# Optimization experiments

Measured on AMD Instinct MI355X. Metric: run time of the kernel, lower is better.

Reference implementation:

```python
import jax, jax.numpy as jnp
import numpy as np


def _rbf(X1, X2, log_ls):
    # exp(-||x1-x2||^2 / (2*ls^2)) via the squared-norm expansion
    sq1 = jnp.sum(X1 * X1, axis=-1)[:, None]
    sq2 = jnp.sum(X2 * X2, axis=-1)[None, :]
    d2 = jnp.maximum(sq1 + sq2 - 2.0 * (X1 @ X2.T), 0.0)
    ls2 = jnp.exp(2.0 * log_ls)
    return jnp.exp(-d2 / (2.0 * ls2))


def setup_inputs() -> dict:
    key = jax.random.key(0)
    k1, k2, k3 = jax.random.split(key, 3)
    N_way, K_shot, Q_query, D = 16, 32, 4096, 1024
    Zs = jax.random.normal(k1, (N_way * K_shot, D), dtype=jnp.float32)
    Ys = jax.random.randint(k2, (N_way * K_shot, 1), 0, N_way)
    Zq = jax.random.normal(k3, (N_way * Q_query, D), dtype=jnp.float32)
    log_ls = jnp.asarray(0.0, dtype=jnp.float32)
    log_noise = jnp.asarray(-3.0, dtype=jnp.float32)
    return {"Zs": Zs, "Ys": Ys, "Zq": Zq, "log_ls": log_ls,
            "log_noise": log_noise, "N_way": N_way}


def reference(Zs, Ys, Zq, log_ls, log_noise, N_way):
    Nsamp = Zs.shape[0]  # N_way * K_shot
    Y1hot = jax.nn.one_hot(Ys.reshape(-1), N_way, dtype=Zs.dtype)  # [Nsamp, N_way]
    noise = jnp.exp(2.0 * log_noise)
    Kss = _rbf(Zs, Zs, log_ls) + noise * jnp.eye(Nsamp, dtype=Zs.dtype)
    L = jnp.linalg.cholesky(Kss)
    alpha = jax.scipy.linalg.cho_solve((L, True), Y1hot)  # [Nsamp, N_way]
    Kqs = _rbf(Zq, Zs, log_ls)  # [Q, Nsamp]
    f_q = Kqs @ alpha  # [Q, N_way]
    return jax.nn.softmax(f_q, axis=-1)
```

## Files before the change

kernel.cpp:

```cpp
#include <hip/hip_runtime.h>
#include <math.h>

#define NS 512
#define NQ 65536
#define DD 1024
#define NW 16

typedef __attribute__((ext_vector_type(8))) short short8x;
typedef __attribute__((ext_vector_type(4))) float floatx4;

static __device__ __forceinline__ unsigned short bf_trunc(float x) {
  return (unsigned short)(__float_as_uint(x) >> 16);
}
static __device__ __forceinline__ float bf_tof(unsigned short h) {
  return __uint_as_float(((unsigned)h) << 16);
}
static __device__ __forceinline__ unsigned short bf_rne(float x) {
  unsigned u = __float_as_uint(x);
  return (unsigned short)((u + 0x7FFFu + ((u >> 16) & 1u)) >> 16);
}

#define STASH(Hp, Lp, row, k0, v) do {                                      \
    unsigned e_ = (unsigned)((((row) * 32 + (k0)) ^ (((row) & 7) << 3)));   \
    ushort4 h_, l_;                                                         \
    h_.x = bf_trunc((v).x); l_.x = bf_trunc((v).x - bf_tof(h_.x));          \
    h_.y = bf_trunc((v).y); l_.y = bf_trunc((v).y - bf_tof(h_.y));          \
    h_.z = bf_trunc((v).z); l_.z = bf_trunc((v).z - bf_tof(h_.z));          \
    h_.w = bf_trunc((v).w); l_.w = bf_trunc((v).w - bf_tof(h_.w));          \
    *(ushort4*)&Hp[e_] = h_; *(ushort4*)&Lp[e_] = l_;                       \
  } while (0)

__global__ void row_norms_kernel(const float* __restrict__ X, float* __restrict__ out, int nrows) {
  int gw = (int)((blockIdx.x * blockDim.x + threadIdx.x) >> 6);
  int lane = threadIdx.x & 63;
  if (gw >= nrows) return;
  const float* row = X + (size_t)gw * DD;
  float s = 0.f;
  #pragma unroll
  for (int i = 0; i < 4; ++i) {
    float4 v = *(const float4*)(row + 4 * lane + 256 * i);
    s += v.x * v.x + v.y * v.y + v.z * v.z + v.w * v.w;
  }
  #pragma unroll
  for (int off = 32; off; off >>= 1) s += __shfl_xor(s, off);
  if (lane == 0) out[gw] = s;
}

__global__ __launch_bounds__(256) void kss_kernel(const float* __restrict__ Zs,
                                                  const float* __restrict__ sn,
                                                  const float* __restrict__ log_ls,
                                                  const float* __restrict__ log_noise,
                                                  float* __restrict__ K) {
  __shared__ __align__(16) float At[16][68];
  __shared__ __align__(16) float Bt[16][68];
  int tid = threadIdx.x;
  int rb = blockIdx.y * 64, cb = blockIdx.x * 64;
  int tx = tid & 15, ty = tid >> 4;
  int srow = tid & 63, skq = (tid >> 6) << 2;
  float acc[4][4] = {};
  for (int kk = 0; kk < DD; kk += 16) {
    __syncthreads();
    float4 a = *(const float4*)(Zs + (size_t)(rb + srow) * DD + kk + skq);
    float4 b = *(const float4*)(Zs + (size_t)(cb + srow) * DD + kk + skq);
    At[skq + 0][srow] = a.x; At[skq + 1][srow] = a.y; At[skq + 2][srow] = a.z; At[skq + 3][srow] = a.w;
    Bt[skq + 0][srow] = b.x; Bt[skq + 1][srow] = b.y; Bt[skq + 2][srow] = b.z; Bt[skq + 3][srow] = b.w;
    __syncthreads();
    #pragma unroll
    for (int k = 0; k < 16; ++k) {
      float4 av = *(const float4*)&At[k][ty * 4];
      float4 bv = *(const float4*)&Bt[k][tx * 4];
      float aa[4] = {av.x, av.y, av.z, av.w};
      float bb[4] = {bv.x, bv.y, bv.z, bv.w};
      #pragma unroll
      for (int i = 0; i < 4; ++i)
        #pragma unroll
        for (int j = 0; j < 4; ++j)
          acc[i][j] = fmaf(aa[i], bb[j], acc[i][j]);
    }
  }
  float inv2 = 0.5f * expf(-2.f * log_ls[0]);
  float noise = expf(2.f * log_noise[0]);
  #pragma unroll
  for (int i = 0; i < 4; ++i)
    #pragma unroll
    for (int j = 0; j < 4; ++j) {
      int r = rb + ty * 4 + i, c = cb + tx * 4 + j;
      float d2 = fmaxf(sn[r] + sn[c] - 2.f * acc[i][j], 0.f);
      float v = expf(-d2 * inv2);
      if (r == c) v += noise;
      K[(size_t)r * NS + c] = v;
    }
}

__global__ __launch_bounds__(512) void chol_panel(float* __restrict__ K, int j) {
  __shared__ float A[64][65];
  __shared__ float diag[64], idia[64];
  int tid = threadIdx.x;
  for (int i = tid; i < 4096; i += 512) {
    int r = i >> 6, c = i & 63;
    A[r][c] = K[(size_t)(j + r) * NS + j + c];
  }
  __syncthreads();
  for (int c = 0; c < 64; ++c) {
    float d = A[c][c];
    float s = sqrtf(d);
    float inv = 1.f / s;
    if (tid == c) { diag[c] = s; idia[c] = inv; }
    if (tid < 64 && tid > c) A[tid][c] *= inv;
    __syncthreads();
    for (int i = tid; i < 4096; i += 512) {
      int r = i >> 6, k = i & 63;
      if (r > c && k > c) A[r][k] -= A[r][c] * A[k][c];
    }
    __syncthreads();
  }
  for (int i = tid; i < 4096; i += 512) {
    int r = i >> 6, c = i & 63;
    if (c <= r) K[(size_t)(j + r) * NS + j + c] = (c == r) ? diag[r] : A[r][c];
  }
  for (int r0 = j + 64 + tid; r0 < NS; r0 += 512) {
    float x[64];
    #pragma unroll
    for (int c = 0; c < 64; ++c) {
      float v = K[(size_t)r0 * NS + j + c];
      #pragma unroll
      for (int k = 0; k < c; ++k) v -= x[k] * A[c][k];
      x[c] = v * idia[c];
    }
    #pragma unroll
    for (int c = 0; c < 64; ++c) K[(size_t)r0 * NS + j + c] = x[c];
  }
}

__global__ __launch_bounds__(256) void syrk_trailing(float* __restrict__ K, int j) {
  int t0 = j + 64;
  int rbt = t0 + blockIdx.y * 64, cbt = t0 + blockIdx.x * 64;
  if (cbt > rbt) return;
  __shared__ float A[64][69];
  __shared__ float B[64][69];
  int tid = threadIdx.x;
  for (int i = tid; i < 64 * 64; i += 256) {
    int r = i >> 6, k = i & 63;
    A[r][k] = K[(size_t)(rbt + r) * NS + j + k];
    B[r][k] = K[(size_t)(cbt + r) * NS + j + k];
  }
  __syncthreads();
  int tx = tid & 15, ty = tid >> 4;
  float acc[4][4] = {};
  for (int k = 0; k < 64; ++k) {
    float aa[4], bb[4];
    #pragma unroll
    for (int i = 0; i < 4; ++i) aa[i] = A[ty * 4 + i][k];
    #pragma unroll
    for (int i = 0; i < 4; ++i) bb[i] = B[tx * 4 + i][k];
    #pragma unroll
    for (int i = 0; i < 4; ++i)
      #pragma unroll
      for (int jj = 0; jj < 4; ++jj)
        acc[i][jj] = fmaf(aa[i], bb[jj], acc[i][jj]);
  }
  #pragma unroll
  for (int i = 0; i < 4; ++i)
    #pragma unroll
    for (int jj = 0; jj < 4; ++jj)
      K[(size_t)(rbt + ty * 4 + i) * NS + cbt + tx * 4 + jj] -= acc[i][jj];
}

__global__ __launch_bounds__(256) void transpose_fill(float* __restrict__ K) {
  int bx = blockIdx.x, by = blockIdx.y;
  if (by < bx) return;
  int rb = by * 64, cb = bx * 64;
  __shared__ float T[64][65];
  int tid = threadIdx.x;
  int rr = tid >> 4, pc = (tid & 15) * 4;
  #pragma unroll
  for (int u = 0; u < 4; ++u) {
    int r = rr + 16 * u;
    *(float4*)&T[r][pc] = *(const float4*)(K + (size_t)(rb + r) * NS + cb + pc);
  }
  __syncthreads();
  if (by == bx) {
    #pragma unroll
    for (int u = 0; u < 4; ++u) {
      int r = rr + 16 * u;
      #pragma unroll
      for (int i = 0; i < 4; ++i) {
        int c = pc + i;
        if (c > r) K[(size_t)(rb + r) * NS + cb + c] = T[c][r];
      }
    }
  } else {
    #pragma unroll
    for (int u = 0; u < 4; ++u) {
      int orr = rr + 16 * u;
      float4 o;
      o.x = T[pc + 0][orr]; o.y = T[pc + 1][orr];
      o.z = T[pc + 2][orr]; o.w = T[pc + 3][orr];
      *(float4*)(K + (size_t)(cb + orr) * NS + rb + pc) = o;
    }
  }
}

__global__ __launch_bounds__(1024) void cho_solve_v2(const float* __restrict__ K,
                                                     const int* __restrict__ Ys,
                                                     unsigned short* __restrict__ alpha_t) {
  __shared__ float P[64][68];
  __shared__ float WsT[16][68];
  __shared__ float Wblk[64][16];
  __shared__ float invd[64];
  const int tid = threadIdx.x;
  const int rs = tid >> 4, nn = tid & 15;
  const int pc = nn * 4;

  float w[8];
  #pragma unroll
  for (int k = 0; k < 8; ++k) w[k] = (Ys[rs + 64 * k] == nn) ? 1.f : 0.f;

  for (int jb = 0; jb < 8; ++jb) {
    const int j = jb << 6;
    __syncthreads();
    #pragma unroll
    for (int k = 0; k < 8; ++k) if (k == jb) Wblk[rs][nn] = w[k];
    *(floatx4*)&P[rs][pc] = *(const floatx4*)(K + (size_t)(j + rs) * NS + j + pc);
    __syncthreads();
    if (tid < 64) {
      const int n = tid & 15, rq = tid >> 4;
      invd[tid] = 1.f / P[tid][tid];
      float w16[16];
      #pragma unroll
      for (int i = 0; i < 16; ++i) w16[i] = Wblk[rq + 4 * i][n];
      #pragma unroll
      for (int g = 0; g < 16; ++g) {
        floatx4 p[16];
        #pragma unroll
        for (int i = 0; i < 16; ++i) p[i] = *(const floatx4*)&P[rq + 4 * i][4 * g];
        #pragma unroll
        for (int cj = 0; cj < 4; ++cj) {
          const int c = 4 * g + cj;
          float xc = __shfl(w16[c >> 2], ((c & 3) << 4) + n) * invd[c];
          if (rq == (c & 3)) w16[c >> 2] = xc;
          #pragma unroll
          for (int i = 0; i < 16; ++i) {
            int r = rq + 4 * i;
            if (r > c) w16[i] -= p[i][cj] * xc;
          }
        }
      }
      #pragma unroll
      for (int i = 0; i < 16; ++i) WsT[n][rq + 4 * i] = w16[i];
    }
    __syncthreads();
    #pragma unroll
    for (int k = 0; k < 8; ++k) if (k == jb) w[k] = WsT[nn][rs];
    floatx4 wsr[16];
    #pragma unroll
    for (int g = 0; g < 16; ++g) wsr[g] = *(const floatx4*)&WsT[nn][4 * g];
    #pragma unroll
    for (int k = 0; k < 8; ++k) {
      if (k > jb) {
        const float* lrow = K + (size_t)(rs + 64 * k) * NS + j;
        float s = w[k];
        #pragma unroll
        for (int g = 0; g < 16; ++g) {
          floatx4 lv = *(const floatx4*)(lrow + 4 * g);
          s -= lv.x * wsr[g].x + lv.y * wsr[g].y + lv.z * wsr[g].z + lv.w * wsr[g].w;
        }
        w[k] = s;
      }
    }
  }

  for (int jb = 7; jb >= 0; --jb) {
    const int j = jb << 6;
    __syncthreads();
    #pragma unroll
    for (int k = 0; k < 8; ++k) if (k == jb) Wblk[rs][nn] = w[k];
    *(floatx4*)&P[rs][pc] = *(const floatx4*)(K + (size_t)(j + rs) * NS + j + pc);
    __syncthreads();
    if (tid < 64) {
      const int n = tid & 15, rq = tid >> 4;
      invd[tid] = 1.f / P[tid][tid];
      float w16[16];
      #pragma unroll
      for (int i = 0; i < 16; ++i) w16[i] = Wblk[rq + 4 * i][n];
      #pragma unroll
      for (int g = 15; g >= 0; --g) {
        floatx4 p[16];
        #pragma unroll
        for (int i = 0; i < 16; ++i) p[i] = *(const floatx4*)&P[rq + 4 * i][4 * g];
        #pragma unroll
        for (int cj = 3; cj >= 0; --cj) {
          const int c = 4 * g + cj;
          float xc = __shfl(w16[c >> 2], ((c & 3) << 4) + n) * invd[c];
          if (rq == (c & 3)) w16[c >> 2] = xc;
          #pragma unroll
          for (int i = 0; i < 16; ++i) {
            int r = rq + 4 * i;
            if (r < c) w16[i] -= p[i][cj] * xc;
          }
        }
      }
      #pragma unroll
      for (int i = 0; i < 16; ++i) WsT[n][rq + 4 * i] = w16[i];
    }
    __syncthreads();
    #pragma unroll
    for (int k = 0; k < 8; ++k) if (k == jb) w[k] = WsT[nn][rs];
    floatx4 wsr[16];
    #pragma unroll
    for (int g = 0; g < 16; ++g) wsr[g] = *(const floatx4*)&WsT[nn][4 * g];
    #pragma unroll
    for (int k = 0; k < 8; ++k) {
      if (k < jb) {
        const float* lrow = K + (size_t)(rs + 64 * k) * NS + j;
        float s = w[k];
        #pragma unroll
        for (int g = 0; g < 16; ++g) {
          floatx4 lv = *(const floatx4*)(lrow + 4 * g);
          s -= lv.x * wsr[g].x + lv.y * wsr[g].y + lv.z * wsr[g].z + lv.w * wsr[g].w;
        }
        w[k] = s;
      }
    }
  }

  #pragma unroll
  for (int k = 0; k < 8; ++k)
    alpha_t[(size_t)nn * NS + rs + 64 * k] = bf_rne(w[k]);
}

__global__ __launch_bounds__(512) void fused_v2(const float* __restrict__ Zq,
                                                const float* __restrict__ Zs,
                                                const float* __restrict__ sn,
                                                const unsigned short* __restrict__ alpha_t,
                                                const float* __restrict__ log_ls,
                                                float* __restrict__ out) {
  __shared__ __align__(16) unsigned short LB[32768];
  __shared__ float qnl[128];
  __shared__ float snl[256];
  unsigned short* AhB = LB;
  unsigned short* AlB = LB + 4096;
  unsigned short* BhB = LB + 8192;
  unsigned short* BlB = LB + 16384;
  unsigned short* KqB = LB;

  const int tid = threadIdx.x;
  const int lane = tid & 63;
  const int w = tid >> 6;
  const int wm = w >> 2, wn = w & 3;
  const int l15 = lane & 15, l4 = lane >> 4;
  const int rb = blockIdx.x * 128;
  const float inv2 = 0.5f * __expf(-2.f * log_ls[0]);
  const unsigned swz = (unsigned)((l15 & 7) << 3);

  if (tid < 128) qnl[tid] = 0.f;
  __syncthreads();

  const int qrow0 = tid >> 3;
  const int qk0 = (tid & 7) * 4;
  const int qrow1 = 64 + qrow0;

  floatx4 facc = {0.f, 0.f, 0.f, 0.f};

  for (int cc = 0; cc < NS; cc += 256) {
    if (tid < 256) snl[tid] = sn[cc + tid];
    floatx4 acc[4][4];
    #pragma unroll
    for (int a = 0; a < 4; ++a)
      #pragma unroll
      for (int b = 0; b < 4; ++b) acc[a][b] = (floatx4){0.f, 0.f, 0.f, 0.f};

    float4 pq0 = *(const float4*)(Zq + (size_t)(rb + qrow0) * DD + qk0);
    float4 pq1 = *(const float4*)(Zq + (size_t)(rb + qrow1) * DD + qk0);
    float4 ps[4];
    #pragma unroll
    for (int u = 0; u < 4; ++u) {
      int idx = tid + (u << 9);
      ps[u] = *(const float4*)(Zs + (size_t)(cc + (idx >> 3)) * DD + ((idx & 7) * 4));
    }

    for (int kt = 0; kt < 32; ++kt) {
      STASH(AhB, AlB, qrow0, qk0, pq0);
      STASH(AhB, AlB, qrow1, qk0, pq1);
      #pragma unroll
      for (int u = 0; u < 4; ++u) {
        int idx = tid + (u << 9);
        int srow = idx >> 3, sk0 = (idx & 7) * 4;
        STASH(BhB, BlB, srow, sk0, ps[u]);
      }
      if (cc == 0) {
        float s0 = pq0.x * pq0.x + pq0.y * pq0.y + pq0.z * pq0.z + pq0.w * pq0.w;
        float s1 = pq1.x * pq1.x + pq1.y * pq1.y + pq1.z * pq1.z + pq1.w * pq1.w;
        #pragma unroll
        for (int d = 1; d < 8; d <<= 1) { s0 += __shfl_xor(s0, d); s1 += __shfl_xor(s1, d); }
        if ((tid & 7) == 0) { qnl[qrow0] += s0; qnl[qrow1] += s1; }
      }
      __syncthreads();
      if (kt < 31) {
        int kk2 = (kt + 1) << 5;
        pq0 = *(const float4*)(Zq + (size_t)(rb + qrow0) * DD + kk2 + qk0);
        pq1 = *(const float4*)(Zq + (size_t)(rb + qrow1) * DD + kk2 + qk0);
        #pragma unroll
        for (int u = 0; u < 4; ++u) {
          int idx = tid + (u << 9);
          ps[u] = *(const float4*)(Zs + (size_t)(cc + (idx >> 3)) * DD + kk2 + ((idx & 7) * 4));
        }
      }
      short8x ah[4], al[4], bh[4], bl[4];
      #pragma unroll
      for (int mi = 0; mi < 4; ++mi) {
        unsigned e = (unsigned)((wm * 64 + mi * 16 + l15) * 32 + 8 * l4) ^ swz;
        ah[mi] = *(const short8x*)&AhB[e];
        al[mi] = *(const short8x*)&AlB[e];
      }
      #pragma unroll
      for (int ni = 0; ni < 4; ++ni) {
        unsigned e = (unsigned)((wn * 64 + ni * 16 + l15) * 32 + 8 * l4) ^ swz;
        bh[ni] = *(const short8x*)&BhB[e];
        bl[ni] = *(const short8x*)&BlB[e];
      }
      #pragma unroll
      for (int mi = 0; mi < 4; ++mi)
        #pragma unroll
        for (int ni = 0; ni < 4; ++ni) {
          acc[mi][ni] = __builtin_amdgcn_mfma_f32_16x16x32_bf16(ah[mi], bh[ni], acc[mi][ni], 0, 0, 0);
          acc[mi][ni] = __builtin_amdgcn_mfma_f32_16x16x32_bf16(ah[mi], bl[ni], acc[mi][ni], 0, 0, 0);
          acc[mi][ni] = __builtin_amdgcn_mfma_f32_16x16x32_bf16(al[mi], bh[ni], acc[mi][ni], 0, 0, 0);
        }
      __syncthreads();
    }

    short8x bfr[8];
    #pragma unroll
    for (int s = 0; s < 8; ++s)
      bfr[s] = *(const short8x*)(alpha_t + ((size_t)l15 * NS + cc + 32 * s + 8 * l4));

    #pragma unroll
    for (int mi = 0; mi < 4; ++mi)
      #pragma unroll
      for (int rr = 0; rr < 4; ++rr) {
        int row_l = wm * 64 + mi * 16 + l4 * 4 + rr;
        float qv = qnl[row_l];
        unsigned sw = (unsigned)((row_l & 7) << 3);
        #pragma unroll
        for (int ni = 0; ni < 4; ++ni) {
          int col = wn * 64 + ni * 16 + l15;
          float d2 = fmaxf(qv + snl[col] - 2.f * acc[mi][ni][rr], 0.f);
          float kq = __expf(-d2 * inv2);
          KqB[(unsigned)(row_l * 256 + col) ^ sw] = bf_rne(kq);
        }
      }
    __syncthreads();
    #pragma unroll
    for (int s = 0; s < 8; ++s) {
      unsigned e = (unsigned)((w * 16 + l15) * 256 + 32 * s + 8 * l4) ^ swz;
      short8x ak = *(const short8x*)&KqB[e];
      facc = __builtin_amdgcn_mfma_f32_16x16x32_bf16(ak, bfr[s], facc, 0, 0, 0);
    }
    __syncthreads();
  }

  #pragma unroll
  for (int r = 0; r < 4; ++r) {
    float v = facc[r];
    float m = v;
    #pragma unroll
    for (int d = 1; d < 16; d <<= 1) m = fmaxf(m, __shfl_xor(m, d));
    float e = __expf(v - m);
    float s = e;
    #pragma unroll
    for (int d = 1; d < 16; d <<= 1) s += __shfl_xor(s, d);
    out[(size_t)(rb + w * 16 + l4 * 4 + r) * NW + l15] = e / s;
  }
}

extern "C" void kernel_launch(void* const* d_in, const int* in_sizes, int n_in,
                              void* d_out, int out_size, void* d_ws, size_t ws_size,
                              hipStream_t stream) {
  (void)in_sizes; (void)n_in; (void)out_size; (void)ws_size;
  const float* Zs = (const float*)d_in[0];
  const int*   Ys = (const int*)d_in[1];
  const float* Zq = (const float*)d_in[2];
  const float* log_ls = (const float*)d_in[3];
  const float* log_noise = (const float*)d_in[4];
  float* out = (float*)d_out;

  float* ws = (float*)d_ws;
  float* K  = ws;
  float* sn = ws + (size_t)NS * NS;
  unsigned short* alpha_t = (unsigned short*)(sn + NS);

  row_norms_kernel<<<128, 256, 0, stream>>>(Zs, sn, NS);
  kss_kernel<<<dim3(8, 8), 256, 0, stream>>>(Zs, sn, log_ls, log_noise, K);
  for (int j = 0; j < NS; j += 64) {
    chol_panel<<<1, 512, 0, stream>>>(K, j);
    int rows = NS - j - 64;
    if (rows > 0) {
      int t = rows / 64;
      syrk_trailing<<<dim3(t, t), 256, 0, stream>>>(K, j);
    }
  }
  transpose_fill<<<dim3(8, 8), 256, 0, stream>>>(K);
  cho_solve_v2<<<1, 1024, 0, stream>>>(K, Ys, alpha_t);
  fused_v2<<<NQ / 128, 512, 0, stream>>>(Zq, Zs, sn, alpha_t, log_ls, out);
}
```

Before: 1.404 ms.

## Fuse blocked Cholesky, trailing update, transpose and solve into one single-block kernel

Replaces the per-panel chol_panel/syrk_trailing launch sequence, the transpose_fill pass and the separate solve with one 1024-thread single-block kernel. The diagonal factorization is done by one wavefront using register rows and shuffles, and the transposed upper triangle is written as it is produced. This removes about 17 kernel launches and their gaps. In exchange, the trailing SYRK updates now run serially on a single CU instead of across many blocks, and they are tightly synchronized.

Result: slower. 1.570 ms (+11.8%).

```diff
diff --git a/kernel.cpp b/kernel.cpp
--- a/kernel.cpp
+++ b/kernel.cpp
@@ -92,126 +92,108 @@
     }
 }
 
-__global__ __launch_bounds__(512) void chol_panel(float* __restrict__ K, int j) {
-  __shared__ float A[64][65];
-  __shared__ float diag[64], idia[64];
-  int tid = threadIdx.x;
-  for (int i = tid; i < 4096; i += 512) {
-    int r = i >> 6, c = i & 63;
-    A[r][c] = K[(size_t)(j + r) * NS + j + c];
-  }
-  __syncthreads();
-  for (int c = 0; c < 64; ++c) {
-    float d = A[c][c];
-    float s = sqrtf(d);
-    float inv = 1.f / s;
-    if (tid == c) { diag[c] = s; idia[c] = inv; }
-    if (tid < 64 && tid > c) A[tid][c] *= inv;
-    __syncthreads();
-    for (int i = tid; i < 4096; i += 512) {
-      int r = i >> 6, k = i & 63;
-      if (r > c && k > c) A[r][k] -= A[r][c] * A[k][c];
-    }
-    __syncthreads();
-  }
-  for (int i = tid; i < 4096; i += 512) {
-    int r = i >> 6, c = i & 63;
-    if (c <= r) K[(size_t)(j + r) * NS + j + c] = (c == r) ? diag[r] : A[r][c];
-  }
-  for (int r0 = j + 64 + tid; r0 < NS; r0 += 512) {
-    float x[64];
-    #pragma unroll
-    for (int c = 0; c < 64; ++c) {
-      float v = K[(size_t)r0 * NS + j + c];
-      #pragma unroll
-      for (int k = 0; k < c; ++k) v -= x[k] * A[c][k];
-      x[c] = v * idia[c];
-    }
-    #pragma unroll
-    for (int c = 0; c < 64; ++c) K[(size_t)r0 * NS + j + c] = x[c];
-  }
-}
-
-__global__ __launch_bounds__(256) void syrk_trailing(float* __restrict__ K, int j) {
-  int t0 = j + 64;
-  int rbt = t0 + blockIdx.y * 64, cbt = t0 + blockIdx.x * 64;
-  if (cbt > rbt) return;
-  __shared__ float A[64][69];
-  __shared__ float B[64][69];
-  int tid = threadIdx.x;
-  for (int i = tid; i < 64 * 64; i += 256) {
-    int r = i >> 6, k = i & 63;
-    A[r][k] = K[(size_t)(rbt + r) * NS + j + k];
-    B[r][k] = K[(size_t)(cbt + r) * NS + j + k];
-  }
-  __syncthreads();
-  int tx = tid & 15, ty = tid >> 4;
-  float acc[4][4] = {};
-  for (int k = 0; k < 64; ++k) {
-    float aa[4], bb[4];
-    #pragma unroll
-    for (int i = 0; i < 4; ++i) aa[i] = A[ty * 4 + i][k];
-    #pragma unroll
-    for (int i = 0; i < 4; ++i) bb[i] = B[tx * 4 + i][k];
-    #pragma unroll
-    for (int i = 0; i < 4; ++i)
-      #pragma unroll
-      for (int jj = 0; jj < 4; ++jj)
-        acc[i][jj] = fmaf(aa[i], bb[jj], acc[i][jj]);
-  }
-  #pragma unroll
-  for (int i = 0; i < 4; ++i)
-    #pragma unroll
-    for (int jj = 0; jj < 4; ++jj)
-      K[(size_t)(rbt + ty * 4 + i) * NS + cbt + tx * 4 + jj] -= acc[i][jj];
-}
-
-__global__ __launch_bounds__(256) void transpose_fill(float* __restrict__ K) {
-  int bx = blockIdx.x, by = blockIdx.y;
-  if (by < bx) return;
-  int rb = by * 64, cb = bx * 64;
-  __shared__ float T[64][65];
-  int tid = threadIdx.x;
-  int rr = tid >> 4, pc = (tid & 15) * 4;
-  #pragma unroll
-  for (int u = 0; u < 4; ++u) {
-    int r = rr + 16 * u;
-    *(float4*)&T[r][pc] = *(const float4*)(K + (size_t)(rb + r) * NS + cb + pc);
-  }
-  __syncthreads();
-  if (by == bx) {
-    #pragma unroll
-    for (int u = 0; u < 4; ++u) {
-      int r = rr + 16 * u;
-      #pragma unroll
-      for (int i = 0; i < 4; ++i) {
-        int c = pc + i;
-        if (c > r) K[(size_t)(rb + r) * NS + cb + c] = T[c][r];
-      }
-    }
-  } else {
-    #pragma unroll
-    for (int u = 0; u < 4; ++u) {
-      int orr = rr + 16 * u;
-      float4 o;
-      o.x = T[pc + 0][orr]; o.y = T[pc + 1][orr];
-      o.z = T[pc + 2][orr]; o.w = T[pc + 3][orr];
-      *(float4*)(K + (size_t)(cb + orr) * NS + rb + pc) = o;
-    }
-  }
-}
-
-__global__ __launch_bounds__(1024) void cho_solve_v2(const float* __restrict__ K,
-                                                     const int* __restrict__ Ys,
-                                                     unsigned short* __restrict__ alpha_t) {
+__global__ __launch_bounds__(1024) void chol_all(float* __restrict__ K,
+                                                 const int* __restrict__ Ys,
+                                                 unsigned short* __restrict__ alpha_t) {
+  __shared__ float A[64][68];
+  __shared__ float SA[64][65];
+  __shared__ float SBt[64][68];
+  __shared__ float idia[64];
   __shared__ float P[64][68];
   __shared__ float WsT[16][68];
   __shared__ float Wblk[64][16];
   __shared__ float invd[64];
   const int tid = threadIdx.x;
+
+  for (int jb = 0; jb < 8; ++jb) {
+    const int j = jb << 6;
+    __syncthreads();
+    if (tid < 64) {
+      const int r = tid;
+      float ar[64];
+      #pragma unroll
+      for (int c4 = 0; c4 < 16; ++c4)
+        *(floatx4*)&ar[c4 * 4] = *(const floatx4*)(K + (size_t)(j + r) * NS + j + c4 * 4);
+      float myinv = 0.f;
+      #pragma unroll
+      for (int c = 0; c < 64; ++c) {
+        float colv = ar[c];
+        float d = __shfl(colv, c);
+        float sq = sqrtf(d);
+        float inv = 1.f / sq;
+        float x = (r > c) ? colv * inv : ((r == c) ? sq : 0.f);
+        ar[c] = x;
+        if (r == c) myinv = inv;
+        #pragma unroll
+        for (int k = c + 1; k < 64; ++k) {
+          float xk = __shfl(x, k);
+          ar[k] = fmaf(-x, xk, ar[k]);
+        }
+      }
+      idia[r] = myinv;
+      #pragma unroll
+      for (int c = 0; c < 64; ++c) {
+        if (c <= r) {
+          A[r][c] = ar[c];
+          K[(size_t)(j + r) * NS + j + c] = ar[c];
+        }
+        if (c < r) K[(size_t)(j + c) * NS + j + r] = ar[c];
+      }
+    }
+    __syncthreads();
+    {
+      const int r0 = j + 64 + tid;
+      if (r0 < NS) {
+        float x[64];
+        #pragma unroll
+        for (int c = 0; c < 64; ++c) {
+          float v = K[(size_t)r0 * NS + j + c];
+          #pragma unroll
+          for (int k = 0; k < c; ++k) v = fmaf(-x[k], A[c][k], v);
+          x[c] = v * idia[c];
+        }
+        #pragma unroll
+        for (int c = 0; c < 64; ++c) {
+          K[(size_t)r0 * NS + j + c] = x[c];
+          K[(size_t)(j + c) * NS + r0] = x[c];
+        }
+      }
+    }
+    const int T = 7 - jb;
+    for (int ti = 0; ti < T; ++ti)
+      for (int tj = 0; tj <= ti; ++tj) {
+        const int rbt = j + 64 + ti * 64, cbt = j + 64 + tj * 64;
+        __syncthreads();
+        {
+          const int rr = tid >> 4, k4 = (tid & 15) * 4;
+          floatx4 av = *(const floatx4*)(K + (size_t)(rbt + rr) * NS + j + k4);
+          floatx4 bv = *(const floatx4*)(K + (size_t)(cbt + rr) * NS + j + k4);
+          SA[rr][k4 + 0] = av.x; SA[rr][k4 + 1] = av.y;
+          SA[rr][k4 + 2] = av.z; SA[rr][k4 + 3] = av.w;
+          SBt[k4 + 0][rr] = bv.x; SBt[k4 + 1][rr] = bv.y;
+          SBt[k4 + 2][rr] = bv.z; SBt[k4 + 3][rr] = bv.w;
+        }
+        __syncthreads();
+        {
+          const int ty = tid & 63, cg = tid >> 6;
+          floatx4 acc = {0.f, 0.f, 0.f, 0.f};
+          #pragma unroll 8
+          for (int k = 0; k < 64; ++k) {
+            float a = SA[ty][k];
+            floatx4 b = *(const floatx4*)&SBt[k][cg * 4];
+            acc.x = fmaf(a, b.x, acc.x); acc.y = fmaf(a, b.y, acc.y);
+            acc.z = fmaf(a, b.z, acc.z); acc.w = fmaf(a, b.w, acc.w);
+          }
+          float* cp = K + (size_t)(rbt + ty) * NS + cbt + cg * 4;
+          floatx4 cv = *(const floatx4*)cp;
+          cv.x -= acc.x; cv.y -= acc.y; cv.z -= acc.z; cv.w -= acc.w;
+          *(floatx4*)cp = cv;
+        }
+      }
+  }
+
   const int rs = tid >> 4, nn = tid & 15;
   const int pc = nn * 4;
-
   float w[8];
   #pragma unroll
   for (int k = 0; k < 8; ++k) w[k] = (Ys[rs + 64 * k] == nn) ? 1.f : 0.f;
@@ -492,15 +474,6 @@
 
   row_norms_kernel<<<128, 256, 0, stream>>>(Zs, sn, NS);
   kss_kernel<<<dim3(8, 8), 256, 0, stream>>>(Zs, sn, log_ls, log_noise, K);
-  for (int j = 0; j < NS; j += 64) {
-    chol_panel<<<1, 512, 0, stream>>>(K, j);
-    int rows = NS - j - 64;
-    if (rows > 0) {
-      int t = rows / 64;
-      syrk_trailing<<<dim3(t, t), 256, 0, stream>>>(K, j);
-    }
-  }
-  transpose_fill<<<dim3(8, 8), 256, 0, stream>>>(K);
-  cho_solve_v2<<<1, 1024, 0, stream>>>(K, Ys, alpha_t);
+  chol_all<<<1, 1024, 0, stream>>>(K, Ys, alpha_t);
   fused_v2<<<NQ / 128, 512, 0, stream>>>(Zq, Zs, sn, alpha_t, log_ls, out);
 }
```

## Rewrite Cholesky panel with wavefront shuffles and fuse transpose fill

Applied to the files above, without the earlier changes.

The 64x64 diagonal block factorization now runs in registers within a single 64-lane wavefront, broadcasting columns with shuffles instead of two block barriers per column. The row triangular solve is blocked by four, reading L from padded shared memory with vector loads. Each panel also writes the upper-triangle mirror directly, so the separate transpose_fill kernel launch is removed. This costs strided transposed global stores, and the 64-float register arrays may raise register pressure.

Measured after the change: 1.478 ms. 5.3% more time.

```diff
diff --git a/kernel.cpp b/kernel.cpp
--- a/kernel.cpp
+++ b/kernel.cpp
@@ -92,43 +92,80 @@
     }
 }
 
-__global__ __launch_bounds__(512) void chol_panel(float* __restrict__ K, int j) {
-  __shared__ float A[64][65];
-  __shared__ float diag[64], idia[64];
-  int tid = threadIdx.x;
-  for (int i = tid; i < 4096; i += 512) {
-    int r = i >> 6, c = i & 63;
-    A[r][c] = K[(size_t)(j + r) * NS + j + c];
+__global__ __launch_bounds__(256) void panel_v2(float* __restrict__ K, int j) {
+  __shared__ float Ld[64][68];
+  __shared__ float idia_s[64];
+  const int tid = threadIdx.x;
+
+  if (tid < 64) {
+    const int r = tid;
+    float ar[64];
+    #pragma unroll
+    for (int c4 = 0; c4 < 16; ++c4)
+      *(floatx4*)&ar[c4 * 4] = *(const floatx4*)(K + (size_t)(j + r) * NS + j + c4 * 4);
+    float myinv = 0.f;
+    #pragma unroll
+    for (int c = 0; c < 64; ++c) {
+      float colv = ar[c];
+      float d = __shfl(colv, c);
+      float sq = sqrtf(d);
+      float inv = 1.f / sq;
+      float x = (r > c) ? colv * inv : ((r == c) ? sq : 0.f);
+      ar[c] = x;
+      if (r == c) myinv = inv;
+      #pragma unroll
+      for (int k = c + 1; k < 64; ++k) {
+        float xk = __shfl(x, k);
+        ar[k] = fmaf(-x, xk, ar[k]);
+      }
+    }
+    idia_s[r] = myinv;
+    #pragma unroll
+    for (int c4 = 0; c4 < 16; ++c4)
+      *(floatx4*)&Ld[r][c4 * 4] = *(const floatx4*)&ar[c4 * 4];
+    #pragma unroll
+    for (int c = 0; c < 64; ++c) {
+      if (c <= r) K[(size_t)(j + r) * NS + j + c] = ar[c];
+      if (c < r)  K[(size_t)(j + c) * NS + j + r] = ar[c];
+    }
   }
   __syncthreads();
-  for (int c = 0; c < 64; ++c) {
-    float d = A[c][c];
-    float s = sqrtf(d);
-    float inv = 1.f / s;
-    if (tid == c) { diag[c] = s; idia[c] = inv; }
-    if (tid < 64 && tid > c) A[tid][c] *= inv;
-    __syncthreads();
-    for (int i = tid; i < 4096; i += 512) {
-      int r = i >> 6, k = i & 63;
-      if (r > c && k > c) A[r][k] -= A[r][c] * A[k][c];
-    }
-    __syncthreads();
-  }
-  for (int i = tid; i < 4096; i += 512) {
-    int r = i >> 6, c = i & 63;
-    if (c <= r) K[(size_t)(j + r) * NS + j + c] = (c == r) ? diag[r] : A[r][c];
-  }
-  for (int r0 = j + 64 + tid; r0 < NS; r0 += 512) {
-    float x[64];
-    #pragma unroll
-    for (int c = 0; c < 64; ++c) {
-      float v = K[(size_t)r0 * NS + j + c];
-      #pragma unroll
-      for (int k = 0; k < c; ++k) v -= x[k] * A[c][k];
-      x[c] = v * idia[c];
-    }
-    #pragma unroll
-    for (int c = 0; c < 64; ++c) K[(size_t)r0 * NS + j + c] = x[c];
+
+  for (int r0 = j + 64 + tid; r0 < NS; r0 += 256) {
+    float xr[64];
+    #pragma unroll
+    for (int c4 = 0; c4 < 16; ++c4)
+      *(floatx4*)&xr[c4 * 4] = *(const floatx4*)(K + (size_t)r0 * NS + j + c4 * 4);
+    #pragma unroll
+    for (int g = 0; g < 16; ++g) {
+      float v0 = xr[4 * g + 0], v1 = xr[4 * g + 1], v2 = xr[4 * g + 2], v3 = xr[4 * g + 3];
+      for (int kb = 0; kb < g; ++kb) {
+        floatx4 x4 = *(const floatx4*)&xr[4 * kb];
+        floatx4 l0 = *(const floatx4*)&Ld[4 * g + 0][4 * kb];
+        floatx4 l1 = *(const floatx4*)&Ld[4 * g + 1][4 * kb];
+        floatx4 l2 = *(const floatx4*)&Ld[4 * g + 2][4 * kb];
+        floatx4 l3 = *(const floatx4*)&Ld[4 * g + 3][4 * kb];
+        v0 -= x4.x * l0.x + x4.y * l0.y + x4.z * l0.z + x4.w * l0.w;
+        v1 -= x4.x * l1.x + x4.y * l1.y + x4.z * l1.z + x4.w * l1.w;
+        v2 -= x4.x * l2.x + x4.y * l2.y + x4.z * l2.z + x4.w * l2.w;
+        v3 -= x4.x * l3.x + x4.y * l3.y + x4.z * l3.z + x4.w * l3.w;
+      }
+      const int c0 = 4 * g;
+      float x0 = v0 * idia_s[c0 + 0];
+      v1 -= x0 * Ld[c0 + 1][c0];
+      float x1 = v1 * idia_s[c0 + 1];
+      v2 -= x0 * Ld[c0 + 2][c0] + x1 * Ld[c0 + 2][c0 + 1];
+      float x2 = v2 * idia_s[c0 + 2];
+      v3 -= x0 * Ld[c0 + 3][c0] + x1 * Ld[c0 + 3][c0 + 1] + x2 * Ld[c0 + 3][c0 + 2];
+      float x3 = v3 * idia_s[c0 + 3];
+      xr[c0 + 0] = x0; xr[c0 + 1] = x1; xr[c0 + 2] = x2; xr[c0 + 3] = x3;
+    }
+    #pragma unroll
+    for (int c4 = 0; c4 < 16; ++c4)
+      *(floatx4*)(K + (size_t)r0 * NS + j + c4 * 4) = *(const floatx4*)&xr[c4 * 4];
+    #pragma unroll
+    for (int c = 0; c < 64; ++c)
+      K[(size_t)(j + c) * NS + r0] = xr[c];
   }
 }
 
@@ -164,41 +201,6 @@
     #pragma unroll
     for (int jj = 0; jj < 4; ++jj)
       K[(size_t)(rbt + ty * 4 + i) * NS + cbt + tx * 4 + jj] -= acc[i][jj];
-}
-
-__global__ __launch_bounds__(256) void transpose_fill(float* __restrict__ K) {
-  int bx = blockIdx.x, by = blockIdx.y;
-  if (by < bx) return;
-  int rb = by * 64, cb = bx * 64;
-  __shared__ float T[64][65];
-  int tid = threadIdx.x;
-  int rr = tid >> 4, pc = (tid & 15) * 4;
-  #pragma unroll
-  for (int u = 0; u < 4; ++u) {
-    int r = rr + 16 * u;
-    *(float4*)&T[r][pc] = *(const float4*)(K + (size_t)(rb + r) * NS + cb + pc);
-  }
-  __syncthreads();
-  if (by == bx) {
-    #pragma unroll
-    for (int u = 0; u < 4; ++u) {
-      int r = rr + 16 * u;
-      #pragma unroll
-      for (int i = 0; i < 4; ++i) {
-        int c = pc + i;
-        if (c > r) K[(size_t)(rb + r) * NS + cb + c] = T[c][r];
-      }
-    }
-  } else {
-    #pragma unroll
-    for (int u = 0; u < 4; ++u) {
-      int orr = rr + 16 * u;
-      float4 o;
-      o.x = T[pc + 0][orr]; o.y = T[pc + 1][orr];
-      o.z = T[pc + 2][orr]; o.w = T[pc + 3][orr];
-      *(float4*)(K + (size_t)(cb + orr) * NS + rb + pc) = o;
-    }
-  }
 }
 
 __global__ __launch_bounds__(1024) void cho_solve_v2(const float* __restrict__ K,
@@ -493,14 +495,13 @@
   row_norms_kernel<<<128, 256, 0, stream>>>(Zs, sn, NS);
   kss_kernel<<<dim3(8, 8), 256, 0, stream>>>(Zs, sn, log_ls, log_noise, K);
   for (int j = 0; j < NS; j += 64) {
-    chol_panel<<<1, 512, 0, stream>>>(K, j);
+    panel_v2<<<1, 256, 0, stream>>>(K, j);
     int rows = NS - j - 64;
     if (rows > 0) {
       int t = rows / 64;
       syrk_trailing<<<dim3(t, t), 256, 0, stream>>>(K, j);
     }
   }
-  transpose_fill<<<dim3(8, 8), 256, 0, stream>>>(K);
   cho_solve_v2<<<1, 1024, 0, stream>>>(K, Ys, alpha_t);
   fused_v2<<<NQ / 128, 512, 0, stream>>>(Zq, Zs, sn, alpha_t, log_ls, out);
 }
```
